# Optimization experiments

Hardware: AMD Instinct MI355X
Metric: run time of the kernel (lower is better)

Reference implementation:

```python
import jax, jax.numpy as jnp
import numpy as np

N_NODES = 100000


def setup_inputs() -> dict:
    key = jax.random.key(0)
    k1, k2, k3 = jax.random.split(key, 3)
    emb = jax.random.normal(k1, (N_NODES, 64), dtype=jnp.float32)
    src = jax.random.randint(k2, (1250000,), 0, N_NODES, dtype=jnp.int64)
    dst = jax.random.randint(k3, (1250000,), 0, N_NODES, dtype=jnp.int64)
    return {"emb": emb, "src": src, "dst": dst}


def reference(emb, src, dst):
    # DGL GraphConv(norm='both', weight=False, bias=False):
    #   out = D_in^{-1/2} * A * (D_out^{-1/2} * emb), degrees clamped to >= 1.
    n = emb.shape[0]
    e = src.shape[0]
    ones = jnp.ones((e,), dtype=emb.dtype)
    out_deg = jax.ops.segment_sum(ones, src, num_segments=n)  # out-degree of src nodes
    in_deg = jax.ops.segment_sum(ones, dst, num_segments=n)   # in-degree of dst nodes
    src_norm = jnp.clip(out_deg, 1.0, None) ** -0.5           # [N]
    dst_norm = jnp.clip(in_deg, 1.0, None) ** -0.5            # [N]
    h = emb * src_norm[:, None]                               # [N, D] pre-normalize
    msg = h[src]                                              # [E, D] gather
    agg = jax.ops.segment_sum(msg, dst, num_segments=n)       # [N, D] scatter-add
    return agg * dst_norm[:, None]
```

## Files before the change

### kernel.cpp

```cpp
#include <hip/hip_runtime.h>
#include <hip/hip_fp16.h>

#define NNODES 100000
#define DIM 64
#define TILE 128
#define NTILES ((NNODES + TILE - 1) / TILE)
#define NTPAD 784
#define CAP 2560
#define EPT 16
#define BIN_THREADS 512
#define BIN_CHUNK (BIN_THREADS * EPT)
#define NPAIR 4
#define SN_THREADS 512

__global__ void init_kernel(int* __restrict__ gcur) {
    int i = blockIdx.x * blockDim.x + threadIdx.x;
    if (i < 2 * NTPAD) gcur[i] = 0;
}

__global__ __launch_bounds__(BIN_THREADS) void bin_kernel(
        const int* __restrict__ src, const int* __restrict__ dst,
        int* __restrict__ gcurD, int* __restrict__ gcurS,
        unsigned int* __restrict__ binnedD, unsigned char* __restrict__ binnedSb, int E) {
    __shared__ int histD[NTPAD], histS[NTPAD], baseD[NTPAD], baseS[NTPAD];
    int dv[EPT], sv[EPT];
    unsigned short rD[EPT], rS[EPT];
    int tid = threadIdx.x;
    for (int t = tid; t < NTPAD; t += BIN_THREADS) { histD[t] = 0; histS[t] = 0; }
    __syncthreads();
    int base = blockIdx.x * BIN_CHUNK;
    #pragma unroll
    for (int i = 0; i < EPT; i++) {
        int idx = base + i * BIN_THREADS + tid;
        if (idx < E) {
            int d = dst[idx];
            int s = src[idx];
            dv[i] = d;
            sv[i] = s;
            rD[i] = (unsigned short)atomicAdd(&histD[d >> 7], 1);
            rS[i] = (unsigned short)atomicAdd(&histS[s >> 7], 1);
        }
    }
    __syncthreads();
    for (int t = tid; t < NTPAD; t += BIN_THREADS) {
        int h = histD[t];
        baseD[t] = h ? atomicAdd(&gcurD[t], h) : 0;
        h = histS[t];
        baseS[t] = h ? atomicAdd(&gcurS[t], h) : 0;
    }
    __syncthreads();
    #pragma unroll
    for (int i = 0; i < EPT; i++) {
        int idx = base + i * BIN_THREADS + tid;
        if (idx < E) {
            int d = dv[i];
            int s = sv[i];
            int tD = d >> 7, tS = s >> 7;
            int pD = baseD[tD] + (int)rD[i];
            int pS = baseS[tS] + (int)rS[i];
            if (pD < CAP) binnedD[(size_t)tD * CAP + pD] = ((unsigned)(d & 127) << 17) | (unsigned)s;
            if (pS < CAP) binnedSb[(size_t)tS * CAP + pS] = (unsigned char)(s & 127);
        }
    }
}

__global__ __launch_bounds__(SN_THREADS) void sortnorm_kernel(
        const int* __restrict__ gcurS, const unsigned char* __restrict__ binnedSb,
        const int* __restrict__ gcurD, const unsigned int* __restrict__ binnedD,
        const float* __restrict__ emb, __half* __restrict__ embp,
        int* __restrict__ sortedD, int* __restrict__ offs, int* __restrict__ deg) {
    __shared__ int cnt[TILE];
    __shared__ int cur[TILE];
    __shared__ float norm_s[TILE];
    __shared__ int wsum[2];
    __shared__ int tot_s;
    int t = blockIdx.x, tid = threadIdx.x;
    if (tid < TILE) cnt[tid] = 0;
    __syncthreads();
    {
        int lenS = min(gcurS[t], CAP);
        const unsigned char* segS = binnedSb + (size_t)t * CAP;
        for (int j = tid; j < lenS; j += SN_THREADS)
            atomicAdd(&cnt[segS[j]], 1);
    }
    __syncthreads();
    if (tid < TILE)
        norm_s[tid] = rsqrtf(fmaxf((float)cnt[tid], 1.0f));
    __syncthreads();
    {
        int nrows = min(TILE, NNODES - t * TILE);
        int chunks = nrows * NPAIR;
        size_t ebase = (size_t)t * TILE * DIM;
        for (int i = tid; i < chunks; i += SN_THREADS) {
            int row = i >> 2;
            int pair = i & 3;
            const float* ep = emb + ebase + (size_t)row * DIM + pair * 16;
            float w = norm_s[row];
            float4 a = *(const float4*)(ep);
            float4 b = *(const float4*)(ep + 4);
            float4 c = *(const float4*)(ep + 8);
            float4 d4 = *(const float4*)(ep + 12);
            int gnode = t * TILE + row;
            __half2* o = (__half2*)(embp + ((size_t)pair * (NNODES + 1) + gnode) * 16);
            o[0] = __floats2half2_rn(a.x * w, a.y * w);
            o[1] = __floats2half2_rn(a.z * w, a.w * w);
            o[2] = __floats2half2_rn(b.x * w, b.y * w);
            o[3] = __floats2half2_rn(b.z * w, b.w * w);
            o[4] = __floats2half2_rn(c.x * w, c.y * w);
            o[5] = __floats2half2_rn(c.z * w, c.w * w);
            o[6] = __floats2half2_rn(d4.x * w, d4.y * w);
            o[7] = __floats2half2_rn(d4.z * w, d4.w * w);
        }
        if (t * TILE + tid == NNODES) {
            __half2 z = __floats2half2_rn(0.0f, 0.0f);
            #pragma unroll
            for (int p = 0; p < NPAIR; p++) {
                __half2* o = (__half2*)(embp + ((size_t)p * (NNODES + 1) + NNODES) * 16);
                #pragma unroll
                for (int k = 0; k < 8; k++) o[k] = z;
            }
        }
    }
    __syncthreads();
    if (tid < TILE) cnt[tid] = 0;
    __syncthreads();
    int len = min(gcurD[t], CAP);
    const unsigned int* seg = binnedD + (size_t)t * CAP;
    for (int j = tid; j < len; j += SN_THREADS)
        atomicAdd(&cnt[seg[j] >> 17], 1);
    __syncthreads();
    int v = 0, ex = 0;
    if (tid < TILE) {
        v = cnt[tid];
        int vpad = (v + 7) & ~7;
        int lane = tid & 63, w = tid >> 6;
        int x = vpad;
        #pragma unroll
        for (int off = 1; off < 64; off <<= 1) {
            int y = __shfl_up(x, off, 64);
            if (lane >= off) x += y;
        }
        if (lane == 63) wsum[w] = x;
        __syncthreads();
        int add = (w == 1) ? wsum[0] : 0;
        ex = x - vpad + add;
        cur[tid] = ex;
        if (tid == TILE - 1) tot_s = ex + vpad;
    } else {
        __syncthreads();
    }
    __syncthreads();
    for (int j = tid; j < len; j += SN_THREADS) {
        unsigned int p = seg[j];
        int dl = p >> 17;
        int pos = atomicAdd(&cur[dl], 1);
        if (pos < CAP) sortedD[(size_t)t * CAP + pos] = (int)(p & 0x1FFFF);
    }
    __syncthreads();
    if (tid < TILE) {
        int vpad = (v + 7) & ~7;
        int pe = ex + vpad;
        for (int p = cur[tid]; p < pe && p < CAP; p++) sortedD[(size_t)t * CAP + p] = NNODES;
    }
    for (int k = tot_s + tid; k < CAP; k += SN_THREADS) sortedD[(size_t)t * CAP + k] = NNODES;
    int node = t * TILE + tid;
    if (tid < TILE && node < NNODES) {
        offs[node] = t * CAP + ex;
        deg[node] = v;
    }
}

__global__ __launch_bounds__(256) void agg6_kernel(
        const __half* __restrict__ embp, const int* __restrict__ offs,
        const int* __restrict__ deg, const int* __restrict__ sortedD,
        float* __restrict__ out) {
    int bid = blockIdx.x;
    int pair = bid & 3;
    int g = bid >> 2;
    int wid = threadIdx.x >> 6;
    int lane = threadIdx.x & 63;
    int nodesub = lane >> 3;
    int slot = (lane >> 1) & 3;
    int hl = lane & 1;
    int node = g * 32 + wid * 8 + nodesub;
    if (node >= NNODES) return;
    int m = deg[node];
    int mp = (m + 7) & ~7;
    const int* run = sortedD + offs[node];
    const __half* tbl = embp + (size_t)pair * (NNODES + 1) * 16;
    __half2 hz = __floats2half2_rn(0.0f, 0.0f);
    __half2 h0 = hz, h1 = hz, h2 = hz, h3 = hz;
    for (int j = 0; j < mp; j += 8) {
        int i0 = run[j + slot];
        int i1 = run[j + 4 + slot];
        float4 v0 = *(const float4*)(tbl + ((size_t)i0 << 4) + (hl << 3));
        float4 v1 = *(const float4*)(tbl + ((size_t)i1 << 4) + (hl << 3));
        const __half2* p0 = (const __half2*)&v0;
        const __half2* p1 = (const __half2*)&v1;
        h0 = __hadd2(h0, p0[0]); h1 = __hadd2(h1, p0[1]);
        h2 = __hadd2(h2, p0[2]); h3 = __hadd2(h3, p0[3]);
        h0 = __hadd2(h0, p1[0]); h1 = __hadd2(h1, p1[1]);
        h2 = __hadd2(h2, p1[2]); h3 = __hadd2(h3, p1[3]);
    }
    float2 f0 = __half22float2(h0);
    float2 f1 = __half22float2(h1);
    float2 f2 = __half22float2(h2);
    float2 f3 = __half22float2(h3);
    float a0 = f0.x, a1 = f0.y, a2 = f1.x, a3 = f1.y;
    float a4 = f2.x, a5 = f2.y, a6 = f3.x, a7 = f3.y;
    #pragma unroll
    for (int off = 2; off <= 4; off <<= 1) {
        a0 += __shfl_xor(a0, off);
        a1 += __shfl_xor(a1, off);
        a2 += __shfl_xor(a2, off);
        a3 += __shfl_xor(a3, off);
        a4 += __shfl_xor(a4, off);
        a5 += __shfl_xor(a5, off);
        a6 += __shfl_xor(a6, off);
        a7 += __shfl_xor(a7, off);
    }
    float dn = rsqrtf(fmaxf((float)m, 1.0f));
    if (slot == 0) {
        float* op = out + ((size_t)node << 6) + (pair << 4) + (hl << 3);
        *(float4*)(op) = make_float4(a0 * dn, a1 * dn, a2 * dn, a3 * dn);
        *(float4*)(op + 4) = make_float4(a4 * dn, a5 * dn, a6 * dn, a7 * dn);
    }
}

extern "C" void kernel_launch(void* const* d_in, const int* in_sizes, int n_in,
                              void* d_out, int out_size, void* d_ws, size_t ws_size,
                              hipStream_t stream) {
    const float* emb = (const float*)d_in[0];
    const int* src = (const int*)d_in[1];
    const int* dst = (const int*)d_in[2];
    int E = in_sizes[1];
    float* out = (float*)d_out;

    int* gcurD = (int*)d_ws;
    int* gcurS = gcurD + NTPAD;
    unsigned int* binnedD = (unsigned int*)(gcurS + NTPAD);
    int* sortedD = (int*)(binnedD + (size_t)NTILES * CAP);
    unsigned char* binnedSb = (unsigned char*)(sortedD + (size_t)NTILES * CAP);
    int* offs = (int*)(binnedSb + (size_t)NTILES * CAP);
    int* deg = offs + NNODES;
    __half* embp = (__half*)(deg + NNODES);

    init_kernel<<<(2 * NTPAD + 255) / 256, 256, 0, stream>>>(gcurD);

    int bin_blocks = (E + BIN_CHUNK - 1) / BIN_CHUNK;
    bin_kernel<<<bin_blocks, BIN_THREADS, 0, stream>>>(src, dst, gcurD, gcurS, binnedD, binnedSb, E);

    sortnorm_kernel<<<NTILES, SN_THREADS, 0, stream>>>(gcurS, binnedSb, gcurD, binnedD,
                                                       emb, embp, sortedD, offs, deg);

    int ngroups = (NNODES + 31) / 32;
    agg6_kernel<<<ngroups * NPAIR, 256, 0, stream>>>(embp, offs, deg, sortedD, out);
}
```

Before: 88.20 us.

## Replace global atomic binning with per-block local sort and tile-start tables

```diff
diff --git a/kernel.cpp b/kernel.cpp
--- a/kernel.cpp
+++ b/kernel.cpp
@@ -6,6 +6,7 @@
 #define TILE 128
 #define NTILES ((NNODES + TILE - 1) / TILE)
 #define NTPAD 784
+#define TS_STRIDE 785
 #define CAP 2560
 #define EPT 16
 #define BIN_THREADS 512
@@ -13,22 +14,20 @@
 #define NPAIR 4
 #define SN_THREADS 512
 
-__global__ void init_kernel(int* __restrict__ gcur) {
-    int i = blockIdx.x * blockDim.x + threadIdx.x;
-    if (i < 2 * NTPAD) gcur[i] = 0;
-}
-
 __global__ __launch_bounds__(BIN_THREADS) void bin_kernel(
         const int* __restrict__ src, const int* __restrict__ dst,
-        int* __restrict__ gcurD, int* __restrict__ gcurS,
-        unsigned int* __restrict__ binnedD, unsigned char* __restrict__ binnedSb, int E) {
-    __shared__ int histD[NTPAD], histS[NTPAD], baseD[NTPAD], baseS[NTPAD];
+        int* __restrict__ blockD, unsigned char* __restrict__ blockSb,
+        unsigned short* __restrict__ tsD, unsigned short* __restrict__ tsS, int E) {
+    __shared__ int histD[NTPAD], histS[NTPAD];
+    __shared__ int baseD[TS_STRIDE], baseS[TS_STRIDE];
+    __shared__ int wsumD[8], wsumS[8];
     int dv[EPT], sv[EPT];
     unsigned short rD[EPT], rS[EPT];
     int tid = threadIdx.x;
+    int blk = blockIdx.x;
     for (int t = tid; t < NTPAD; t += BIN_THREADS) { histD[t] = 0; histS[t] = 0; }
     __syncthreads();
-    int base = blockIdx.x * BIN_CHUNK;
+    int base = blk * BIN_CHUNK;
     #pragma unroll
     for (int i = 0; i < EPT; i++) {
         int idx = base + i * BIN_THREADS + tid;
@@ -42,46 +41,78 @@
         }
     }
     __syncthreads();
-    for (int t = tid; t < NTPAD; t += BIN_THREADS) {
-        int h = histD[t];
-        baseD[t] = h ? atomicAdd(&gcurD[t], h) : 0;
-        h = histS[t];
-        baseS[t] = h ? atomicAdd(&gcurS[t], h) : 0;
-    }
-    __syncthreads();
+    {
+        int i0 = 2 * tid, i1 = 2 * tid + 1;
+        int aD = (i0 < NTPAD) ? histD[i0] : 0;
+        int bD = (i1 < NTPAD) ? histD[i1] : 0;
+        int aS = (i0 < NTPAD) ? histS[i0] : 0;
+        int bS = (i1 < NTPAD) ? histS[i1] : 0;
+        int vD = aD + bD, vS = aS + bS;
+        int lane = tid & 63, w = tid >> 6;
+        int xD = vD, xS = vS;
+        #pragma unroll
+        for (int off = 1; off < 64; off <<= 1) {
+            int yD = __shfl_up(xD, off, 64);
+            int yS = __shfl_up(xS, off, 64);
+            if (lane >= off) { xD += yD; xS += yS; }
+        }
+        if (lane == 63) { wsumD[w] = xD; wsumS[w] = xS; }
+        __syncthreads();
+        if (tid == 0) {
+            int runD = 0, runS = 0;
+            #pragma unroll
+            for (int k = 0; k < 8; k++) {
+                int tD = wsumD[k]; wsumD[k] = runD; runD += tD;
+                int tS = wsumS[k]; wsumS[k] = runS; runS += tS;
+            }
+            baseD[NTPAD] = runD;
+            baseS[NTPAD] = runS;
+        }
+        __syncthreads();
+        int exD = xD - vD + wsumD[w];
+        int exS = xS - vS + wsumS[w];
+        if (i0 < NTPAD) { baseD[i0] = exD; baseS[i0] = exS; }
+        if (i1 < NTPAD) { baseD[i1] = exD + aD; baseS[i1] = exS + aS; }
+    }
+    __syncthreads();
+    for (int t = tid; t <= NTPAD; t += BIN_THREADS) {
+        tsD[(size_t)blk * TS_STRIDE + t] = (unsigned short)baseD[t];
+        tsS[(size_t)blk * TS_STRIDE + t] = (unsigned short)baseS[t];
+    }
     #pragma unroll
     for (int i = 0; i < EPT; i++) {
         int idx = base + i * BIN_THREADS + tid;
         if (idx < E) {
             int d = dv[i];
             int s = sv[i];
-            int tD = d >> 7, tS = s >> 7;
-            int pD = baseD[tD] + (int)rD[i];
-            int pS = baseS[tS] + (int)rS[i];
-            if (pD < CAP) binnedD[(size_t)tD * CAP + pD] = ((unsigned)(d & 127) << 17) | (unsigned)s;
-            if (pS < CAP) binnedSb[(size_t)tS * CAP + pS] = (unsigned char)(s & 127);
+            int pD = baseD[d >> 7] + (int)rD[i];
+            int pS = baseS[s >> 7] + (int)rS[i];
+            blockD[((size_t)blk << 13) + pD] = ((unsigned)(d & 127) << 17) | (unsigned)s;
+            blockSb[((size_t)blk << 13) + pS] = (unsigned char)(s & 127);
         }
     }
 }
 
 __global__ __launch_bounds__(SN_THREADS) void sortnorm_kernel(
-        const int* __restrict__ gcurS, const unsigned char* __restrict__ binnedSb,
-        const int* __restrict__ gcurD, const unsigned int* __restrict__ binnedD,
-        const float* __restrict__ emb, __half* __restrict__ embp,
+        const int* __restrict__ blockD, const unsigned char* __restrict__ blockSb,
+        const unsigned short* __restrict__ tsD, const unsigned short* __restrict__ tsS,
+        int nblk, const float* __restrict__ emb, __half* __restrict__ embp,
         int* __restrict__ sortedD, int* __restrict__ offs, int* __restrict__ deg) {
     __shared__ int cnt[TILE];
     __shared__ int cur[TILE];
     __shared__ float norm_s[TILE];
-    __shared__ int wsum[2];
-    __shared__ int tot_s;
+    __shared__ int wsum[8];
+    __shared__ int gtot_s, tot_s;
+    __shared__ int ebuf[CAP];
     int t = blockIdx.x, tid = threadIdx.x;
     if (tid < TILE) cnt[tid] = 0;
     __syncthreads();
-    {
-        int lenS = min(gcurS[t], CAP);
-        const unsigned char* segS = binnedSb + (size_t)t * CAP;
-        for (int j = tid; j < lenS; j += SN_THREADS)
-            atomicAdd(&cnt[segS[j]], 1);
+    if (tid < nblk) {
+        const unsigned short* ts = tsS + (size_t)tid * TS_STRIDE;
+        int s0 = ts[t], s1 = ts[t + 1];
+        const unsigned char* seg = blockSb + ((size_t)tid << 13);
+        for (int j = s0; j < s1; j++)
+            atomicAdd(&cnt[seg[j]], 1);
     }
     __syncthreads();
     if (tid < TILE)
@@ -122,12 +153,44 @@
         }
     }
     __syncthreads();
+    int n = 0, s0 = 0;
+    if (tid < nblk) {
+        const unsigned short* ts = tsD + (size_t)tid * TS_STRIDE;
+        s0 = ts[t];
+        n = ts[t + 1] - s0;
+    }
+    {
+        int lane = tid & 63, w = tid >> 6;
+        int x = n;
+        #pragma unroll
+        for (int off = 1; off < 64; off <<= 1) {
+            int y = __shfl_up(x, off, 64);
+            if (lane >= off) x += y;
+        }
+        if (lane == 63) wsum[w] = x;
+        __syncthreads();
+        if (tid == 0) {
+            int run = 0;
+            #pragma unroll
+            for (int k = 0; k < 8; k++) { int tt = wsum[k]; wsum[k] = run; run += tt; }
+            gtot_s = run;
+        }
+        __syncthreads();
+        int pos = x - n + wsum[w];
+        if (tid < nblk) {
+            const int* sp = blockD + ((size_t)tid << 13) + s0;
+            for (int k = 0; k < n; k++) {
+                int p = pos + k;
+                if (p < CAP) ebuf[p] = sp[k];
+            }
+        }
+    }
+    __syncthreads();
+    int len = min(gtot_s, CAP);
     if (tid < TILE) cnt[tid] = 0;
     __syncthreads();
-    int len = min(gcurD[t], CAP);
-    const unsigned int* seg = binnedD + (size_t)t * CAP;
     for (int j = tid; j < len; j += SN_THREADS)
-        atomicAdd(&cnt[seg[j] >> 17], 1);
+        atomicAdd(&cnt[((unsigned)ebuf[j]) >> 17], 1);
     __syncthreads();
     int v = 0, ex = 0;
     if (tid < TILE) {
@@ -151,7 +214,7 @@
     }
     __syncthreads();
     for (int j = tid; j < len; j += SN_THREADS) {
-        unsigned int p = seg[j];
+        unsigned int p = (unsigned)ebuf[j];
         int dl = p >> 17;
         int pos = atomicAdd(&cur[dl], 1);
         if (pos < CAP) sortedD[(size_t)t * CAP + pos] = (int)(p & 0x1FFFF);
@@ -236,21 +299,26 @@
     int E = in_sizes[1];
     float* out = (float*)d_out;
 
-    int* gcurD = (int*)d_ws;
-    int* gcurS = gcurD + NTPAD;
-    unsigned int* binnedD = (unsigned int*)(gcurS + NTPAD);
-    int* sortedD = (int*)(binnedD + (size_t)NTILES * CAP);
-    unsigned char* binnedSb = (unsigned char*)(sortedD + (size_t)NTILES * CAP);
-    int* offs = (int*)(binnedSb + (size_t)NTILES * CAP);
-    int* deg = offs + NNODES;
-    __half* embp = (__half*)(deg + NNODES);
-
-    init_kernel<<<(2 * NTPAD + 255) / 256, 256, 0, stream>>>(gcurD);
-
-    int bin_blocks = (E + BIN_CHUNK - 1) / BIN_CHUNK;
-    bin_kernel<<<bin_blocks, BIN_THREADS, 0, stream>>>(src, dst, gcurD, gcurS, binnedD, binnedSb, E);
-
-    sortnorm_kernel<<<NTILES, SN_THREADS, 0, stream>>>(gcurS, binnedSb, gcurD, binnedD,
+    int nblk = (E + BIN_CHUNK - 1) / BIN_CHUNK;
+    char* p = (char*)d_ws;
+    auto align16 = [](char* q) { return (char*)(((uintptr_t)q + 15) & ~(uintptr_t)15); };
+
+    int* blockD = (int*)p;                 p += (size_t)nblk * BIN_CHUNK * 4;
+    unsigned char* blockSb = (unsigned char*)p;  p += (size_t)nblk * BIN_CHUNK;
+    p = align16(p);
+    unsigned short* tsD = (unsigned short*)p;    p += (size_t)nblk * TS_STRIDE * 2;
+    p = align16(p);
+    unsigned short* tsS = (unsigned short*)p;    p += (size_t)nblk * TS_STRIDE * 2;
+    p = align16(p);
+    int* sortedD = (int*)p;                p += (size_t)NTILES * CAP * 4;
+    int* offs = (int*)p;                   p += (size_t)NNODES * 4;
+    int* deg = (int*)p;                    p += (size_t)NNODES * 4;
+    p = align16(p);
+    __half* embp = (__half*)p;
+
+    bin_kernel<<<nblk, BIN_THREADS, 0, stream>>>(src, dst, blockD, blockSb, tsD, tsS, E);
+
+    sortnorm_kernel<<<NTILES, SN_THREADS, 0, stream>>>(blockD, blockSb, tsD, tsS, nblk,
                                                        emb, embp, sortedD, offs, deg);
 
     int ngroups = (NNODES + 31) / 32;
```

After: 90.71 us. 1.03x slower.
